# Kernel tuning notes

Hardware: AMD Instinct MI355X
Metric: run time of the kernel (lower is better)

## Reference

```python
import jax, jax.numpy as jnp
import numpy as np

# config constants (init_kwargs)
WC, WS = 0.5, 0.5            # boundary cosine / structural weights (hybrid mode)
TARGET_BPP = 6.0             # target_bytes_per_patch
GAIN = 1.0                   # target_patch_gain
THRESH = 0.5                 # boundary_threshold; mask = p >= THRESH
EPS = 1e-6

_POP6 = jnp.array([bin(i).count('1') for i in range(64)], dtype=jnp.int32)

def _pop6(x):
    return _POP6[jnp.clip(x, 0, 63)]

def _logit(p):
    p = jnp.clip(p, EPS, 1.0 - EPS)
    return jnp.log(p) - jnp.log1p(-p)

def _next(x):  # shift-left by one, zero-padded at end (matches torch q_next pattern)
    return jnp.concatenate([x[1:], jnp.zeros((1,), x.dtype)])

def _hist(vals, mask, bins):
    idx = jnp.where(mask, vals, bins)  # invalid -> out of range, dropped
    return jnp.zeros((bins,), jnp.int32).at[idx].add(1, mode='drop')


def setup_inputs() -> dict:
    key = jax.random.key(0)
    ks = jax.random.split(key, 6)
    B, S = 4, 1048576
    return {
        'boundary_logprobs': jax.random.normal(ks[0], (B, S), jnp.float32),
        'states': jax.random.randint(ks[1], (B, S), 0, 4096, jnp.int32),
        'q_class': jax.random.randint(ks[2], (B, S), 0, 64, jnp.int32),
        'family': jax.random.randint(ks[3], (B, S), 0, 4, jnp.int32),
        'micro_ref': jax.random.randint(ks[4], (B, S), 0, 64, jnp.int32),
        'valid_mask': jax.random.randint(ks[5], (B, S), 0, 2, jnp.int32).astype(bool),
    }


def reference(boundary_logprobs, states, q_class, family, micro_ref, valid_mask):
    B, S = valid_mask.shape
    v = valid_mask.reshape(-1)
    st = states.reshape(-1).astype(jnp.int32)
    q = q_class.reshape(-1).astype(jnp.int32)
    fam = family.reshape(-1).astype(jnp.int32)
    mic = micro_ref.reshape(-1).astype(jnp.int32)

    # --- structural boundary probs ---
    omega12 = st & 0xFFF
    c6 = ((omega12 >> 6) ^ omega12) & 63          # chirality6
    d_chi = jnp.clip(_pop6(c6 ^ _next(c6)).astype(jnp.float32) / 6.0, 0.0, 1.0)
    d_q = _pop6((q & 63) ^ (_next(q) & 63)).astype(jnp.float32) / 6.0
    fx = (fam & 3) ^ (_next(fam) & 3)
    d_fam = (((fx & 1) != 0).astype(jnp.float32) + ((fx & 2) != 0).astype(jnp.float32)) / 2.0
    score = jnp.clip(0.5 * d_chi + 0.35 * d_q + 0.15 * d_fam, EPS, 1.0)
    structural = jnp.where(v, score, 0.0)

    # --- combine with cosine probs (hybrid mode) ---
    cosine = jnp.exp(jnp.minimum(boundary_logprobs.reshape(-1), 0.0))
    combined = (WC * cosine + WS * structural) / max(WC + WS, 1e-6)

    # --- target bytes-per-patch rate adjustment ---
    vf = v.astype(jnp.float32)
    vc = jnp.maximum(jnp.sum(vf), 1.0)
    cur = jnp.clip(jnp.sum(combined * vf) / vc, 1e-4, 1.0 - 1e-4)
    tgt = max(1e-4, min(1.0 - 1e-4, 1.0 / TARGET_BPP))
    shift = _logit(jnp.asarray(tgt, jnp.float32)) - _logit(cur)
    combined = jax.nn.sigmoid(_logit(combined) + GAIN * shift)
    combined = jnp.clip(combined, EPS, 1.0 - EPS)
    combined_logprobs = jnp.log(combined)
    bmask = combined_logprobs >= jnp.log(jnp.asarray(THRESH, jnp.float32))

    # --- histograms over effective (valid) positions ---
    shell = _pop6(c6)
    q_hist64 = _hist(q, v, 64)
    family_hist4 = _hist(fam, v, 4)
    micro_hist64 = _hist(mic, v, 64)
    shell_hist7 = _hist(shell, v, 7)
    wt_q = _pop6(q & 63)
    q_weight_hist7 = _hist(wt_q, v, 7)
    bits = ((q & 63)[:, None] >> jnp.arange(6)) & 1            # [n, 6]
    bit_excitation6 = jnp.sum(bits * v[:, None].astype(jnp.int32), axis=0)

    # --- patch lengths (vectorized run-length over valid bytes) ---
    bv = bmask & v
    pos = jnp.cumsum(v.astype(jnp.int32))                      # 1-indexed valid position
    bpos = jnp.where(bv, pos, 0)
    prev = jax.lax.cummax(jnp.concatenate([jnp.zeros((1,), jnp.int32), bpos[:-1]]))
    lengths = jnp.where(bv, pos - prev, 0)                     # dense run lengths at boundaries
    total_valid = pos[-1]
    trailing = total_valid - jax.lax.cummax(bpos)[-1]          # open trailing run
    patch_count = jnp.sum(bv).astype(jnp.int32) + (trailing > 0).astype(jnp.int32)

    return (combined_logprobs.reshape(B, S), bmask.reshape(B, S), structural.reshape(B, S),
            q_hist64, family_hist4, micro_hist64, shell_hist7, q_weight_hist7,
            bit_excitation6, lengths, trailing, patch_count)
```

## Files before the change

kernel.cpp:

```cpp
#include <hip/hip_runtime.h>

#define TPB 256
#define EPT 8
#define CHUNK (TPB * EPT)
#define NSLICE 64

typedef unsigned long long ull;
typedef long long ll;

__device__ __forceinline__ ull shfl_down_u64(ull x, int off) {
    unsigned lo = (unsigned)x, hi = (unsigned)(x >> 32);
    lo = __shfl_down(lo, off, 64);
    hi = __shfl_down(hi, off, 64);
    return ((ull)hi << 32) | lo;
}

__global__ __launch_bounds__(TPB, 8) void k_passA(
    const float* __restrict__ blp, const int* __restrict__ st,
    const int* __restrict__ q, const int* __restrict__ fam,
    const int* __restrict__ mic, const int* __restrict__ vm,
    float* __restrict__ out_structural,
    int* __restrict__ ghist, ull* __restrict__ lookA,
    int* __restrict__ pos_offset, float* __restrict__ shiftp,
    int* __restrict__ totalv_p, int n)
{
    __shared__ int lh2[2048];
    __shared__ int slhs[11];
    __shared__ int swv[4];
    __shared__ float swc[4];

    const int tid = threadIdx.x, lane = tid & 63, wave = tid >> 6;
    const long i0 = (long)blockIdx.x * CHUNK + (long)tid * EPT;
    const bool fast = ((long)(blockIdx.x + 1) * CHUNK <= n);

    int stv[9], qv[9], fv[9], micv[8], vmv[8];
    float bpv[8];
    if (fast) {
        const int4 sa = *(const int4*)(st + i0),  sb = *(const int4*)(st + i0 + 4);
        const int4 qa = *(const int4*)(q + i0),   qb = *(const int4*)(q + i0 + 4);
        const int4 fa = *(const int4*)(fam + i0), fb = *(const int4*)(fam + i0 + 4);
        const int4 ma = *(const int4*)(mic + i0), mb = *(const int4*)(mic + i0 + 4);
        const int4 va = *(const int4*)(vm + i0),  vb = *(const int4*)(vm + i0 + 4);
        const float4 ba = *(const float4*)(blp + i0), bb = *(const float4*)(blp + i0 + 4);
        int nst = __shfl_down(sa.x, 1, 64);
        int nq  = __shfl_down(qa.x, 1, 64);
        int nf  = __shfl_down(fa.x, 1, 64);
        if (lane == 63) {
            const long j = i0 + 8;
            nst = (j < n) ? st[j]  : 0;
            nq  = (j < n) ? q[j]   : 0;
            nf  = (j < n) ? fam[j] : 0;
        }
        stv[0]=sa.x; stv[1]=sa.y; stv[2]=sa.z; stv[3]=sa.w; stv[4]=sb.x; stv[5]=sb.y; stv[6]=sb.z; stv[7]=sb.w; stv[8]=nst;
        qv[0]=qa.x;  qv[1]=qa.y;  qv[2]=qa.z;  qv[3]=qa.w;  qv[4]=qb.x;  qv[5]=qb.y;  qv[6]=qb.z;  qv[7]=qb.w;  qv[8]=nq;
        fv[0]=fa.x;  fv[1]=fa.y;  fv[2]=fa.z;  fv[3]=fa.w;  fv[4]=fb.x;  fv[5]=fb.y;  fv[6]=fb.z;  fv[7]=fb.w;  fv[8]=nf;
        micv[0]=ma.x; micv[1]=ma.y; micv[2]=ma.z; micv[3]=ma.w; micv[4]=mb.x; micv[5]=mb.y; micv[6]=mb.z; micv[7]=mb.w;
        vmv[0]=va.x; vmv[1]=va.y; vmv[2]=va.z; vmv[3]=va.w; vmv[4]=vb.x; vmv[5]=vb.y; vmv[6]=vb.z; vmv[7]=vb.w;
        bpv[0]=ba.x; bpv[1]=ba.y; bpv[2]=ba.z; bpv[3]=ba.w; bpv[4]=bb.x; bpv[5]=bb.y; bpv[6]=bb.z; bpv[7]=bb.w;
    } else {
        #pragma unroll
        for (int e = 0; e < 8; ++e) {
            long ii = i0 + e;
            bool r = ii < n;
            stv[e] = r ? st[ii] : 0;  qv[e] = r ? q[ii] : 0;  fv[e] = r ? fam[ii] : 0;
            micv[e] = r ? mic[ii] : 0; vmv[e] = r ? vm[ii] : 0; bpv[e] = r ? blp[ii] : 0.f;
        }
        stv[8] = (i0 + 8 < n) ? st[i0 + 8] : 0;
        qv[8]  = (i0 + 8 < n) ? q[i0 + 8] : 0;
        fv[8]  = (i0 + 8 < n) ? fam[i0 + 8] : 0;
    }

    {
        int4 z4; z4.x = 0; z4.y = 0; z4.z = 0; z4.w = 0;
        *(int4*)&lh2[tid * 8] = z4;
        *(int4*)&lh2[tid * 8 + 4] = z4;
    }
    if (tid < 11) slhs[tid] = 0;
    __syncthreads();

    const int qrow = ((wave << 2) | (lane & 3)) << 6;
    int sv = 0;
    float scf = 0.0f;
    ull accF = 0, accS0 = 0, accS1 = 0;
    float structural[8];
    #pragma unroll
    for (int e = 0; e < 8; ++e) {
        int sti = stv[e], qi = qv[e], fi = fv[e], mi = micv[e];
        int v = (vmv[e] != 0);
        int om  = sti & 0xFFF;      int c6  = ((om  >> 6) ^ om ) & 63;
        int omn = stv[e+1] & 0xFFF; int c6n = ((omn >> 6) ^ omn) & 63;
        float d_chi = (float)__popc(c6 ^ c6n) * (1.0f / 6.0f);
        float d_q   = (float)__popc((qi & 63) ^ (qv[e+1] & 63)) * (1.0f / 6.0f);
        int fx = (fi & 3) ^ (fv[e+1] & 3);
        float d_fam = (float)((fx & 1) + ((fx >> 1) & 1)) * 0.5f;
        float score = 0.5f * d_chi + 0.35f * d_q + 0.15f * d_fam;
        score = fminf(fmaxf(score, 1e-6f), 1.0f);
        structural[e] = v ? score : 0.0f;
        float cosine = expf(fminf(bpv[e], 0.0f));
        float combined = 0.5f * (cosine + structural[e]);
        if (v) {
            sv += 1;
            scf += combined;
            atomicAdd(&lh2[qrow + (qi & 63)], 1);
            atomicAdd(&lh2[1024 + qrow + (mi & 63)], 1);
            accF += 1ULL << ((fi & 3) * 16);
            int sh = __popc(c6);
            ull ts = 1ULL << ((sh & 3) * 16);
            if (sh < 4) accS0 += ts; else accS1 += ts;
        }
    }

    if (fast) {
        float4 o;
        o.x=structural[0]; o.y=structural[1]; o.z=structural[2]; o.w=structural[3];
        *(float4*)(out_structural + i0) = o;
        o.x=structural[4]; o.y=structural[5]; o.z=structural[6]; o.w=structural[7];
        *(float4*)(out_structural + i0 + 4) = o;
    } else {
        #pragma unroll
        for (int e = 0; e < 8; ++e)
            if (i0 + e < n) out_structural[i0 + e] = structural[e];
    }

    #pragma unroll
    for (int off = 32; off > 0; off >>= 1) {
        sv  += __shfl_down(sv, off, 64);
        scf += __shfl_down(scf, off, 64);
        accF  += shfl_down_u64(accF, off);
        accS0 += shfl_down_u64(accS0, off);
        accS1 += shfl_down_u64(accS1, off);
    }
    if (lane == 0) {
        swv[wave] = sv; swc[wave] = scf;
        #pragma unroll
        for (int b2 = 0; b2 < 4; ++b2) atomicAdd(&slhs[b2],     (int)((accF  >> (16*b2)) & 0xFFFF));
        #pragma unroll
        for (int b2 = 0; b2 < 4; ++b2) atomicAdd(&slhs[4 + b2], (int)((accS0 >> (16*b2)) & 0xFFFF));
        #pragma unroll
        for (int b2 = 0; b2 < 3; ++b2) atomicAdd(&slhs[8 + b2], (int)((accS1 >> (16*b2)) & 0xFFFF));
    }
    __syncthreads();

    if (wave != 0) {
        int t2 = tid - 64;
        if (t2 < 139) {
            int val;
            if (t2 < 64) {
                val = 0;
                #pragma unroll
                for (int r = 0; r < 16; ++r) val += lh2[(r << 6) + t2];
            } else if (t2 < 68) {
                val = slhs[t2 - 64];
            } else if (t2 < 132) {
                int b2 = t2 - 68;
                val = 0;
                #pragma unroll
                for (int r = 0; r < 16; ++r) val += lh2[1024 + (r << 6) + b2];
            } else {
                val = slhs[4 + (t2 - 132)];
            }
            if (val) atomicAdd(&ghist[(blockIdx.x & (NSLICE - 1)) * 152 + t2], val);
        }
    } else {
        const int b = blockIdx.x;
        const ll lv = (ll)(swv[0] + swv[1] + swv[2] + swv[3]);
        const double lcd = (double)swc[0] + (double)swc[1] + (double)swc[2] + (double)swc[3];
        const ll lcf = (ll)(lcd * 16384.0 + 0.5);
        if (lane == 0)
            atomicExch(&lookA[b], (1ULL << 62) | ((ull)lv << 39) | (ull)lcf);
        ll exV = 0, exC = 0;
        int base = b - 1;
        while (base >= 0) {
            int idx = base - lane;
            ull w; int stt;
            for (;;) {
                w = (idx >= 0) ? atomicAdd(&lookA[idx], 0ULL) : (2ULL << 62);
                stt = (int)(w >> 62);
                if (!__ballot(stt == 0)) break;
                __builtin_amdgcn_s_sleep(1);
            }
            ull incm = __ballot(stt == 2);
            int stop = incm ? (__ffsll((ll)incm) - 1) : 64;
            ll v = 0, c = 0;
            if (lane <= stop && idx >= 0) {
                v = (ll)((w >> 39) & 0x7FFFFFULL);
                c = (ll)(w & 0x7FFFFFFFFFULL);
            }
            #pragma unroll
            for (int off = 32; off > 0; off >>= 1) {
                v += (ll)shfl_down_u64((ull)v, off);
                c += (ll)shfl_down_u64((ull)c, off);
            }
            exV += v; exC += c;
            if (stop < 64) break;
            base -= 64;
        }
        if (lane == 0) {
            atomicExch(&lookA[b], (2ULL << 62) | ((ull)(exV + lv) << 39) | (ull)(exC + lcf));
            pos_offset[b] = (int)exV;
            if (b == (int)gridDim.x - 1) {
                int tv = (int)(exV + lv);
                *totalv_p = tv;
                double vc = (double)(tv > 1 ? tv : 1);
                float cur = (float)(((double)(exC + lcf) * (1.0 / 16384.0)) / vc);
                cur = fminf(fmaxf(cur, 1e-4f), 0.9999f);
                float p = fminf(fmaxf(cur, 1e-6f), 0.999999f);
                float lc = logf(p) - log1pf(-p);
                float tgt = (float)(1.0 / 6.0);
                float lt = logf(tgt) - log1pf(-tgt);
                *shiftp = lt - lc;
            }
        }
    }
}

__global__ __launch_bounds__(TPB, 8) void k_passB(
    const float* __restrict__ strc, const float* __restrict__ blp,
    const int* __restrict__ pos_offset, const float* __restrict__ shiftp,
    const int* __restrict__ totalv_p, const int* __restrict__ ghist,
    ull* __restrict__ lookB,
    float* __restrict__ out_logp, float* __restrict__ out_bmask,
    float* __restrict__ out_len, float* __restrict__ out_hist,
    float* __restrict__ out_trailing, float* __restrict__ out_patch, int n)
{
    __shared__ int swt[4], swm[4], scnt[4];
    __shared__ int sCarry;
    __shared__ int qh[64];
    const int tid = threadIdx.x, lane = tid & 63, wave = tid >> 6;
    const long i0 = (long)blockIdx.x * CHUNK + (long)tid * EPT;
    const bool fast = ((long)(blockIdx.x + 1) * CHUNK <= n);

    float sv8[8], bp8[8];
    if (fast) {
        const float4 s0 = *(const float4*)(strc + i0), s1 = *(const float4*)(strc + i0 + 4);
        const float4 p0 = *(const float4*)(blp + i0),  p1 = *(const float4*)(blp + i0 + 4);
        sv8[0]=s0.x; sv8[1]=s0.y; sv8[2]=s0.z; sv8[3]=s0.w; sv8[4]=s1.x; sv8[5]=s1.y; sv8[6]=s1.z; sv8[7]=s1.w;
        bp8[0]=p0.x; bp8[1]=p0.y; bp8[2]=p0.z; bp8[3]=p0.w; bp8[4]=p1.x; bp8[5]=p1.y; bp8[6]=p1.z; bp8[7]=p1.w;
    } else {
        #pragma unroll
        for (int e = 0; e < 8; ++e) {
            long ii = i0 + e;
            bool r = ii < n;
            sv8[e] = r ? strc[ii] : 0.0f;
            bp8[e] = r ? blp[ii] : 0.0f;
        }
    }

    const float shift = *shiftp;
    const int wb0 = pos_offset[blockIdx.x];
    const float K = expf(-shift);

    unsigned mv = 0, mb = 0;
    float lp[8], bmf[8], lenv[8];
    #pragma unroll
    for (int e = 0; e < 8; ++e) {
        float s = sv8[e];
        int v = (s > 0.0f);
        float cosine = expf(fminf(bp8[e], 0.0f));
        float comb = 0.5f * (cosine + s);
        float p = fminf(fmaxf(comb, 1e-6f), 0.999999f);
        float d = fmaf(K, 1.0f - p, p);
        float sgm = p / d;
        sgm = fminf(fmaxf(sgm, 1e-6f), 0.999999f);
        float clp = logf(sgm);
        lp[e] = clp;
        int bm = (clp >= -0.69314718f) ? 1 : 0;
        bmf[e] = (float)bm;
        mv |= (unsigned)v << e;
        if (bm & v) mb |= 1u << e;
        lenv[e] = 0.0f;
    }
    if (fast) {
        float4 o;
        o.x=lp[0]; o.y=lp[1]; o.z=lp[2]; o.w=lp[3];     *(float4*)(out_logp + i0) = o;
        o.x=lp[4]; o.y=lp[5]; o.z=lp[6]; o.w=lp[7];     *(float4*)(out_logp + i0 + 4) = o;
        o.x=bmf[0]; o.y=bmf[1]; o.z=bmf[2]; o.w=bmf[3]; *(float4*)(out_bmask + i0) = o;
        o.x=bmf[4]; o.y=bmf[5]; o.z=bmf[6]; o.w=bmf[7]; *(float4*)(out_bmask + i0 + 4) = o;
    } else {
        #pragma unroll
        for (int e = 0; e < 8; ++e)
            if (i0 + e < n) { out_logp[i0 + e] = lp[e]; out_bmask[i0 + e] = bmf[e]; }
    }

    int tvc = __popc(mv);
    int x = tvc;
    #pragma unroll
    for (int off = 1; off < 64; off <<= 1) {
        int y = __shfl_up(x, off, 64);
        if (lane >= off) x += y;
    }
    if (lane == 63) swt[wave] = x;
    __syncthreads();
    int wb = wb0;
    for (int w2 = 0; w2 < wave; ++w2) wb += swt[w2];
    const int vbase = wb + (x - tvc);

    int last = -1;
    if (mb) {
        int hb = 31 - __clz(mb);
        last = vbase + __popc(mv & ((2u << hb) - 1));
    }
    int m = last;
    #pragma unroll
    for (int off = 1; off < 64; off <<= 1) {
        int y = __shfl_up(m, off, 64);
        if (lane >= off && y > m) m = y;
    }
    int exm = __shfl_up(m, 1, 64);
    if (lane == 0) exm = -1;
    if (lane == 63) swm[wave] = m;
    int cnt = __popc(mb);
    #pragma unroll
    for (int off = 32; off > 0; off >>= 1)
        cnt += __shfl_down(cnt, off, 64);
    if (lane == 0) scnt[wave] = cnt;
    __syncthreads();

    if (wave == 0) {
        const int b = blockIdx.x;
        int Lown = swm[0];
        if (swm[1] > Lown) Lown = swm[1];
        if (swm[2] > Lown) Lown = swm[2];
        if (swm[3] > Lown) Lown = swm[3];
        if (Lown < 0) Lown = 0;
        const ll Cown = (ll)(scnt[0] + scnt[1] + scnt[2] + scnt[3]);
        if (lane == 0)
            atomicExch(&lookB[b], (1ULL << 62) | ((ull)Lown << 23) | (ull)Cown);
        ll exM = 0, exC = 0;
        int base = b - 1;
        while (base >= 0) {
            int idx = base - lane;
            ull w; int stt;
            for (;;) {
                w = (idx >= 0) ? atomicAdd(&lookB[idx], 0ULL) : (2ULL << 62);
                stt = (int)(w >> 62);
                if (!__ballot(stt == 0)) break;
                __builtin_amdgcn_s_sleep(1);
            }
            ull incm = __ballot(stt == 2);
            int stop = incm ? (__ffsll((ll)incm) - 1) : 64;
            ll mm = 0, c = 0;
            if (lane <= stop && idx >= 0) {
                mm = (ll)((w >> 23) & 0x7FFFFFULL);
                c  = (ll)(w & 0x7FFFFFULL);
            }
            #pragma unroll
            for (int off = 32; off > 0; off >>= 1) {
                ll mo = (ll)shfl_down_u64((ull)mm, off);
                if (mo > mm) mm = mo;
                c += (ll)shfl_down_u64((ull)c, off);
            }
            if (mm > exM) exM = mm;
            exC += c;
            if (stop < 64) break;
            base -= 64;
        }
        if (lane == 0) {
            ll incM = exM > (ll)Lown ? exM : (ll)Lown;
            atomicExch(&lookB[b], (2ULL << 62) | ((ull)incM << 23) | (ull)(exC + Cown));
            sCarry = (int)exM;
            if (b == (int)gridDim.x - 1) {
                int tv = *totalv_p;
                int trailing = tv - (int)incM;
                *out_trailing = (float)trailing;
                *out_patch = (float)((int)(exC + Cown) + (trailing > 0 ? 1 : 0));
            }
        }
    }
    __syncthreads();

    int prev = sCarry;
    if (exm > prev) prev = exm;
    for (int w2 = 0; w2 < wave; ++w2) if (swm[w2] > prev) prev = swm[w2];
    int runv = 0;
    #pragma unroll
    for (int e = 0; e < 8; ++e) {
        runv += (mv >> e) & 1;
        if ((mb >> e) & 1) {
            int pos = vbase + runv;
            lenv[e] = (float)(pos - prev);
            prev = pos;
        }
    }
    if (fast) {
        float4 o;
        o.x=lenv[0]; o.y=lenv[1]; o.z=lenv[2]; o.w=lenv[3]; *(float4*)(out_len + i0) = o;
        o.x=lenv[4]; o.y=lenv[5]; o.z=lenv[6]; o.w=lenv[7]; *(float4*)(out_len + i0 + 4) = o;
    } else {
        #pragma unroll
        for (int e = 0; e < 8; ++e)
            if (i0 + e < n) out_len[i0 + e] = lenv[e];
    }

    if (blockIdx.x == 0) {
        if (tid < 139) {
            int acc = 0;
            #pragma unroll 8
            for (int sl = 0; sl < NSLICE; ++sl) acc += ghist[sl * 152 + tid];
            out_hist[tid] = (float)acc;
            if (tid < 64) qh[tid] = acc;
        }
        __syncthreads();
        if (tid < 7) {
            int sacc = 0;
            for (int b = 0; b < 64; ++b) if (__popc(b) == tid) sacc += qh[b];
            out_hist[139 + tid] = (float)sacc;
        }
        if (tid < 6) {
            int sacc = 0;
            for (int b = 0; b < 64; ++b) sacc += qh[b] * ((b >> tid) & 1);
            out_hist[146 + tid] = (float)sacc;
        }
    }
}

extern "C" void kernel_launch(void* const* d_in, const int* in_sizes, int n_in,
                              void* d_out, int out_size, void* d_ws, size_t ws_size,
                              hipStream_t stream)
{
    const float* blp = (const float*)d_in[0];
    const int* st   = (const int*)d_in[1];
    const int* q    = (const int*)d_in[2];
    const int* fam  = (const int*)d_in[3];
    const int* mic  = (const int*)d_in[4];
    const int* vm   = (const int*)d_in[5];
    const int n = in_sizes[0];
    const int nb = (n + CHUNK - 1) / CHUNK;

    float* out = (float*)d_out;
    float* out_logp       = out;
    float* out_bmask      = out + (size_t)n;
    float* out_structural = out + 2 * (size_t)n;
    float* out_hist       = out + 3 * (size_t)n;
    float* out_len        = out + 3 * (size_t)n + 152;
    float* out_trailing   = out + 4 * (size_t)n + 152;
    float* out_patch      = out + 4 * (size_t)n + 153;

    char* w = (char*)d_ws;
    int*    ghist      = (int*)(w);
    ull*    lookA      = (ull*)(w + 40960);
    ull*    lookB      = (ull*)(w + 57344);
    int*    pos_offset = (int*)(w + 73728);
    float*  shiftp     = (float*)(w + 81920);
    int*    totalv_p   = (int*)(w + 81924);

    hipMemsetAsync(w, 0, 73728, stream);

    k_passA<<<dim3(nb), dim3(TPB), 0, stream>>>(
        blp, st, q, fam, mic, vm, out_structural,
        ghist, lookA, pos_offset, shiftp, totalv_p, n);

    k_passB<<<dim3(nb), dim3(TPB), 0, stream>>>(
        out_structural, blp, pos_offset, shiftp, totalv_p, ghist, lookB,
        out_logp, out_bmask, out_len, out_hist, out_trailing, out_patch, n);
}
```

Baseline: 192.9 us.

## Replace decoupled look-back scans with two-level group aggregates and resize blocks

Pass A's serial decoupled look-back is replaced. Each block now writes a packed per-block partial and atomically adds it into a per-group (32-block) sum. Pass B computes its valid-position offset and the global shift directly from those group sums and in-group partials, so the inter-block chain in pass A goes away. Pass B's max/count scan now uses per-group atomicMax/atomicAdd with a done counter plus in-group partials instead of walking back through lookB. Blocks change from 256 threads × 8 elements to 512 × 4. This cuts the serialized look-back latency, but pass B still spins on other blocks, and it relies on the grid having at most 64 groups.

```diff
diff --git a/kernel.cpp b/kernel.cpp
--- a/kernel.cpp
+++ b/kernel.cpp
@@ -1,9 +1,10 @@
 #include <hip/hip_runtime.h>
 
-#define TPB 256
-#define EPT 8
+#define TPB 512
+#define EPT 4
 #define CHUNK (TPB * EPT)
 #define NSLICE 64
+#define NW 8
 
 typedef unsigned long long ull;
 typedef long long ll;
@@ -20,71 +21,69 @@
     const int* __restrict__ q, const int* __restrict__ fam,
     const int* __restrict__ mic, const int* __restrict__ vm,
     float* __restrict__ out_structural,
-    int* __restrict__ ghist, ull* __restrict__ lookA,
-    int* __restrict__ pos_offset, float* __restrict__ shiftp,
-    int* __restrict__ totalv_p, int n)
+    int* __restrict__ ghist, ull* __restrict__ partialA,
+    ull* __restrict__ l1sumA, int n)
 {
     __shared__ int lh2[2048];
     __shared__ int slhs[11];
-    __shared__ int swv[4];
-    __shared__ float swc[4];
+    __shared__ int swv[NW];
+    __shared__ float swc[NW];
 
     const int tid = threadIdx.x, lane = tid & 63, wave = tid >> 6;
     const long i0 = (long)blockIdx.x * CHUNK + (long)tid * EPT;
     const bool fast = ((long)(blockIdx.x + 1) * CHUNK <= n);
 
-    int stv[9], qv[9], fv[9], micv[8], vmv[8];
-    float bpv[8];
+    int stv[5], qv[5], fv[5], micv[4], vmv[4];
+    float bpv[4];
     if (fast) {
-        const int4 sa = *(const int4*)(st + i0),  sb = *(const int4*)(st + i0 + 4);
-        const int4 qa = *(const int4*)(q + i0),   qb = *(const int4*)(q + i0 + 4);
-        const int4 fa = *(const int4*)(fam + i0), fb = *(const int4*)(fam + i0 + 4);
-        const int4 ma = *(const int4*)(mic + i0), mb = *(const int4*)(mic + i0 + 4);
-        const int4 va = *(const int4*)(vm + i0),  vb = *(const int4*)(vm + i0 + 4);
-        const float4 ba = *(const float4*)(blp + i0), bb = *(const float4*)(blp + i0 + 4);
+        const int4 sa = *(const int4*)(st + i0);
+        const int4 qa = *(const int4*)(q + i0);
+        const int4 fa = *(const int4*)(fam + i0);
+        const int4 ma = *(const int4*)(mic + i0);
+        const int4 va = *(const int4*)(vm + i0);
+        const float4 ba = *(const float4*)(blp + i0);
         int nst = __shfl_down(sa.x, 1, 64);
         int nq  = __shfl_down(qa.x, 1, 64);
         int nf  = __shfl_down(fa.x, 1, 64);
         if (lane == 63) {
-            const long j = i0 + 8;
+            const long j = i0 + 4;
             nst = (j < n) ? st[j]  : 0;
             nq  = (j < n) ? q[j]   : 0;
             nf  = (j < n) ? fam[j] : 0;
         }
-        stv[0]=sa.x; stv[1]=sa.y; stv[2]=sa.z; stv[3]=sa.w; stv[4]=sb.x; stv[5]=sb.y; stv[6]=sb.z; stv[7]=sb.w; stv[8]=nst;
-        qv[0]=qa.x;  qv[1]=qa.y;  qv[2]=qa.z;  qv[3]=qa.w;  qv[4]=qb.x;  qv[5]=qb.y;  qv[6]=qb.z;  qv[7]=qb.w;  qv[8]=nq;
-        fv[0]=fa.x;  fv[1]=fa.y;  fv[2]=fa.z;  fv[3]=fa.w;  fv[4]=fb.x;  fv[5]=fb.y;  fv[6]=fb.z;  fv[7]=fb.w;  fv[8]=nf;
-        micv[0]=ma.x; micv[1]=ma.y; micv[2]=ma.z; micv[3]=ma.w; micv[4]=mb.x; micv[5]=mb.y; micv[6]=mb.z; micv[7]=mb.w;
-        vmv[0]=va.x; vmv[1]=va.y; vmv[2]=va.z; vmv[3]=va.w; vmv[4]=vb.x; vmv[5]=vb.y; vmv[6]=vb.z; vmv[7]=vb.w;
-        bpv[0]=ba.x; bpv[1]=ba.y; bpv[2]=ba.z; bpv[3]=ba.w; bpv[4]=bb.x; bpv[5]=bb.y; bpv[6]=bb.z; bpv[7]=bb.w;
+        stv[0]=sa.x; stv[1]=sa.y; stv[2]=sa.z; stv[3]=sa.w; stv[4]=nst;
+        qv[0]=qa.x;  qv[1]=qa.y;  qv[2]=qa.z;  qv[3]=qa.w;  qv[4]=nq;
+        fv[0]=fa.x;  fv[1]=fa.y;  fv[2]=fa.z;  fv[3]=fa.w;  fv[4]=nf;
+        micv[0]=ma.x; micv[1]=ma.y; micv[2]=ma.z; micv[3]=ma.w;
+        vmv[0]=va.x; vmv[1]=va.y; vmv[2]=va.z; vmv[3]=va.w;
+        bpv[0]=ba.x; bpv[1]=ba.y; bpv[2]=ba.z; bpv[3]=ba.w;
     } else {
         #pragma unroll
-        for (int e = 0; e < 8; ++e) {
+        for (int e = 0; e < 4; ++e) {
             long ii = i0 + e;
             bool r = ii < n;
             stv[e] = r ? st[ii] : 0;  qv[e] = r ? q[ii] : 0;  fv[e] = r ? fam[ii] : 0;
             micv[e] = r ? mic[ii] : 0; vmv[e] = r ? vm[ii] : 0; bpv[e] = r ? blp[ii] : 0.f;
         }
-        stv[8] = (i0 + 8 < n) ? st[i0 + 8] : 0;
-        qv[8]  = (i0 + 8 < n) ? q[i0 + 8] : 0;
-        fv[8]  = (i0 + 8 < n) ? fam[i0 + 8] : 0;
+        stv[4] = (i0 + 4 < n) ? st[i0 + 4] : 0;
+        qv[4]  = (i0 + 4 < n) ? q[i0 + 4] : 0;
+        fv[4]  = (i0 + 4 < n) ? fam[i0 + 4] : 0;
     }
 
     {
         int4 z4; z4.x = 0; z4.y = 0; z4.z = 0; z4.w = 0;
-        *(int4*)&lh2[tid * 8] = z4;
-        *(int4*)&lh2[tid * 8 + 4] = z4;
+        *(int4*)&lh2[tid * 4] = z4;
     }
     if (tid < 11) slhs[tid] = 0;
     __syncthreads();
 
-    const int qrow = ((wave << 2) | (lane & 3)) << 6;
+    const int qrow = ((wave << 1) | (lane & 1)) << 6;
     int sv = 0;
     float scf = 0.0f;
     ull accF = 0, accS0 = 0, accS1 = 0;
-    float structural[8];
-    #pragma unroll
-    for (int e = 0; e < 8; ++e) {
+    float structural[4];
+    #pragma unroll
+    for (int e = 0; e < 4; ++e) {
         int sti = stv[e], qi = qv[e], fi = fv[e], mi = micv[e];
         int v = (vmv[e] != 0);
         int om  = sti & 0xFFF;      int c6  = ((om  >> 6) ^ om ) & 63;
@@ -114,11 +113,9 @@
         float4 o;
         o.x=structural[0]; o.y=structural[1]; o.z=structural[2]; o.w=structural[3];
         *(float4*)(out_structural + i0) = o;
-        o.x=structural[4]; o.y=structural[5]; o.z=structural[6]; o.w=structural[7];
-        *(float4*)(out_structural + i0 + 4) = o;
     } else {
         #pragma unroll
-        for (int e = 0; e < 8; ++e)
+        for (int e = 0; e < 4; ++e)
             if (i0 + e < n) out_structural[i0 + e] = structural[e];
     }
 
@@ -141,122 +138,109 @@
     }
     __syncthreads();
 
-    if (wave != 0) {
-        int t2 = tid - 64;
-        if (t2 < 139) {
-            int val;
-            if (t2 < 64) {
-                val = 0;
-                #pragma unroll
-                for (int r = 0; r < 16; ++r) val += lh2[(r << 6) + t2];
-            } else if (t2 < 68) {
-                val = slhs[t2 - 64];
-            } else if (t2 < 132) {
-                int b2 = t2 - 68;
-                val = 0;
-                #pragma unroll
-                for (int r = 0; r < 16; ++r) val += lh2[1024 + (r << 6) + b2];
-            } else {
-                val = slhs[4 + (t2 - 132)];
-            }
-            if (val) atomicAdd(&ghist[(blockIdx.x & (NSLICE - 1)) * 152 + t2], val);
-        }
-    } else {
-        const int b = blockIdx.x;
-        const ll lv = (ll)(swv[0] + swv[1] + swv[2] + swv[3]);
-        const double lcd = (double)swc[0] + (double)swc[1] + (double)swc[2] + (double)swc[3];
-        const ll lcf = (ll)(lcd * 16384.0 + 0.5);
-        if (lane == 0)
-            atomicExch(&lookA[b], (1ULL << 62) | ((ull)lv << 39) | (ull)lcf);
-        ll exV = 0, exC = 0;
-        int base = b - 1;
-        while (base >= 0) {
-            int idx = base - lane;
-            ull w; int stt;
-            for (;;) {
-                w = (idx >= 0) ? atomicAdd(&lookA[idx], 0ULL) : (2ULL << 62);
-                stt = (int)(w >> 62);
-                if (!__ballot(stt == 0)) break;
-                __builtin_amdgcn_s_sleep(1);
-            }
-            ull incm = __ballot(stt == 2);
-            int stop = incm ? (__ffsll((ll)incm) - 1) : 64;
-            ll v = 0, c = 0;
-            if (lane <= stop && idx >= 0) {
-                v = (ll)((w >> 39) & 0x7FFFFFULL);
-                c = (ll)(w & 0x7FFFFFFFFFULL);
-            }
+    if (tid == 0) {
+        int vsum = 0; double cs = 0.0;
+        #pragma unroll
+        for (int w2 = 0; w2 < NW; ++w2) { vsum += swv[w2]; cs += (double)swc[w2]; }
+        ll cf = (ll)(cs * 16384.0 + 0.5);
+        ull packed = ((ull)(unsigned)vsum << 39) | (ull)cf;
+        partialA[blockIdx.x] = packed;
+        atomicAdd(&l1sumA[blockIdx.x >> 5], packed);
+    }
+    if (tid < 139) {
+        int t2 = tid;
+        int val;
+        if (t2 < 64) {
+            val = 0;
             #pragma unroll
-            for (int off = 32; off > 0; off >>= 1) {
-                v += (ll)shfl_down_u64((ull)v, off);
-                c += (ll)shfl_down_u64((ull)c, off);
-            }
-            exV += v; exC += c;
-            if (stop < 64) break;
-            base -= 64;
-        }
-        if (lane == 0) {
-            atomicExch(&lookA[b], (2ULL << 62) | ((ull)(exV + lv) << 39) | (ull)(exC + lcf));
-            pos_offset[b] = (int)exV;
-            if (b == (int)gridDim.x - 1) {
-                int tv = (int)(exV + lv);
-                *totalv_p = tv;
-                double vc = (double)(tv > 1 ? tv : 1);
-                float cur = (float)(((double)(exC + lcf) * (1.0 / 16384.0)) / vc);
-                cur = fminf(fmaxf(cur, 1e-4f), 0.9999f);
-                float p = fminf(fmaxf(cur, 1e-6f), 0.999999f);
-                float lc = logf(p) - log1pf(-p);
-                float tgt = (float)(1.0 / 6.0);
-                float lt = logf(tgt) - log1pf(-tgt);
-                *shiftp = lt - lc;
-            }
-        }
+            for (int r = 0; r < 16; ++r) val += lh2[(r << 6) + t2];
+        } else if (t2 < 68) {
+            val = slhs[t2 - 64];
+        } else if (t2 < 132) {
+            int b2 = t2 - 68;
+            val = 0;
+            #pragma unroll
+            for (int r = 0; r < 16; ++r) val += lh2[1024 + (r << 6) + b2];
+        } else {
+            val = slhs[4 + (t2 - 132)];
+        }
+        if (val) atomicAdd(&ghist[(blockIdx.x & (NSLICE - 1)) * 152 + t2], val);
     }
 }
 
 __global__ __launch_bounds__(TPB, 8) void k_passB(
     const float* __restrict__ strc, const float* __restrict__ blp,
-    const int* __restrict__ pos_offset, const float* __restrict__ shiftp,
-    const int* __restrict__ totalv_p, const int* __restrict__ ghist,
-    ull* __restrict__ lookB,
+    const ull* __restrict__ partialA, const ull* __restrict__ l1sumA,
+    const int* __restrict__ ghist,
+    ull* __restrict__ partial2, unsigned* __restrict__ l1max2,
+    unsigned* __restrict__ l1cnt2, int* __restrict__ grpdone2,
     float* __restrict__ out_logp, float* __restrict__ out_bmask,
     float* __restrict__ out_len, float* __restrict__ out_hist,
     float* __restrict__ out_trailing, float* __restrict__ out_patch, int n)
 {
-    __shared__ int swt[4], swm[4], scnt[4];
-    __shared__ int sCarry;
+    __shared__ int swt[NW], swm[NW], scnt[NW];
+    __shared__ int sCarry, sTV, sPos0;
+    __shared__ float sShift;
     __shared__ int qh[64];
     const int tid = threadIdx.x, lane = tid & 63, wave = tid >> 6;
     const long i0 = (long)blockIdx.x * CHUNK + (long)tid * EPT;
     const bool fast = ((long)(blockIdx.x + 1) * CHUNK <= n);
-
-    float sv8[8], bp8[8];
+    const int nb = (int)gridDim.x;
+    const int b = (int)blockIdx.x;
+    const int g = b >> 5, r = b & 31;
+
+    float sv4[4], bp4[4];
     if (fast) {
-        const float4 s0 = *(const float4*)(strc + i0), s1 = *(const float4*)(strc + i0 + 4);
-        const float4 p0 = *(const float4*)(blp + i0),  p1 = *(const float4*)(blp + i0 + 4);
-        sv8[0]=s0.x; sv8[1]=s0.y; sv8[2]=s0.z; sv8[3]=s0.w; sv8[4]=s1.x; sv8[5]=s1.y; sv8[6]=s1.z; sv8[7]=s1.w;
-        bp8[0]=p0.x; bp8[1]=p0.y; bp8[2]=p0.z; bp8[3]=p0.w; bp8[4]=p1.x; bp8[5]=p1.y; bp8[6]=p1.z; bp8[7]=p1.w;
+        const float4 s0 = *(const float4*)(strc + i0);
+        const float4 p0 = *(const float4*)(blp + i0);
+        sv4[0]=s0.x; sv4[1]=s0.y; sv4[2]=s0.z; sv4[3]=s0.w;
+        bp4[0]=p0.x; bp4[1]=p0.y; bp4[2]=p0.z; bp4[3]=p0.w;
     } else {
         #pragma unroll
-        for (int e = 0; e < 8; ++e) {
+        for (int e = 0; e < 4; ++e) {
             long ii = i0 + e;
-            bool r = ii < n;
-            sv8[e] = r ? strc[ii] : 0.0f;
-            bp8[e] = r ? blp[ii] : 0.0f;
-        }
-    }
-
-    const float shift = *shiftp;
-    const int wb0 = pos_offset[blockIdx.x];
+            bool r2 = ii < n;
+            sv4[e] = r2 ? strc[ii] : 0.0f;
+            bp4[e] = r2 ? blp[ii] : 0.0f;
+        }
+    }
+
+    if (wave == 0) {
+        ull cell = l1sumA[lane];
+        int vc = (int)(cell >> 39);
+        ll cc = (ll)(cell & ((1ULL << 39) - 1));
+        int vex = (lane < g) ? vc : 0;
+        if (lane < r) vex += (int)(partialA[(g << 5) + lane] >> 39);
+        int vt = vc; ll ct = cc;
+        #pragma unroll
+        for (int off = 32; off > 0; off >>= 1) {
+            vt  += __shfl_down(vt, off, 64);
+            vex += __shfl_down(vex, off, 64);
+            ct  += (ll)shfl_down_u64((ull)ct, off);
+        }
+        if (lane == 0) {
+            sTV = vt; sPos0 = vex;
+            double vcd = (double)(vt > 1 ? vt : 1);
+            float cur = (float)(((double)ct * (1.0 / 16384.0)) / vcd);
+            cur = fminf(fmaxf(cur, 1e-4f), 0.9999f);
+            float p = fminf(fmaxf(cur, 1e-6f), 0.999999f);
+            float lc = logf(p) - log1pf(-p);
+            float tgt = (float)(1.0 / 6.0);
+            float lt = logf(tgt) - log1pf(-tgt);
+            sShift = lt - lc;
+        }
+    }
+    __syncthreads();
+    const float shift = sShift;
     const float K = expf(-shift);
 
     unsigned mv = 0, mb = 0;
-    float lp[8], bmf[8], lenv[8];
-    #pragma unroll
-    for (int e = 0; e < 8; ++e) {
-        float s = sv8[e];
+    float lp[4], bmf[4], lenv[4];
+    #pragma unroll
+    for (int e = 0; e < 4; ++e) {
+        float s = sv4[e];
         int v = (s > 0.0f);
-        float cosine = expf(fminf(bp8[e], 0.0f));
+        float cosine = expf(fminf(bp4[e], 0.0f));
         float comb = 0.5f * (cosine + s);
         float p = fminf(fmaxf(comb, 1e-6f), 0.999999f);
         float d = fmaf(K, 1.0f - p, p);
@@ -273,12 +257,10 @@
     if (fast) {
         float4 o;
         o.x=lp[0]; o.y=lp[1]; o.z=lp[2]; o.w=lp[3];     *(float4*)(out_logp + i0) = o;
-        o.x=lp[4]; o.y=lp[5]; o.z=lp[6]; o.w=lp[7];     *(float4*)(out_logp + i0 + 4) = o;
         o.x=bmf[0]; o.y=bmf[1]; o.z=bmf[2]; o.w=bmf[3]; *(float4*)(out_bmask + i0) = o;
-        o.x=bmf[4]; o.y=bmf[5]; o.z=bmf[6]; o.w=bmf[7]; *(float4*)(out_bmask + i0 + 4) = o;
     } else {
         #pragma unroll
-        for (int e = 0; e < 8; ++e)
+        for (int e = 0; e < 4; ++e)
             if (i0 + e < n) { out_logp[i0 + e] = lp[e]; out_bmask[i0 + e] = bmf[e]; }
     }
 
@@ -291,7 +273,7 @@
     }
     if (lane == 63) swt[wave] = x;
     __syncthreads();
-    int wb = wb0;
+    int wb = sPos0;
     for (int w2 = 0; w2 < wave; ++w2) wb += swt[w2];
     const int vbase = wb + (x - tvc);
 
@@ -317,53 +299,52 @@
     __syncthreads();
 
     if (wave == 0) {
-        const int b = blockIdx.x;
-        int Lown = swm[0];
-        if (swm[1] > Lown) Lown = swm[1];
-        if (swm[2] > Lown) Lown = swm[2];
-        if (swm[3] > Lown) Lown = swm[3];
+        int Lown = swm[0], Cown = scnt[0];
+        #pragma unroll
+        for (int w2 = 1; w2 < NW; ++w2) {
+            if (swm[w2] > Lown) Lown = swm[w2];
+            Cown += scnt[w2];
+        }
         if (Lown < 0) Lown = 0;
-        const ll Cown = (ll)(scnt[0] + scnt[1] + scnt[2] + scnt[3]);
-        if (lane == 0)
-            atomicExch(&lookB[b], (1ULL << 62) | ((ull)Lown << 23) | (ull)Cown);
-        ll exM = 0, exC = 0;
-        int base = b - 1;
-        while (base >= 0) {
-            int idx = base - lane;
-            ull w; int stt;
-            for (;;) {
-                w = (idx >= 0) ? atomicAdd(&lookB[idx], 0ULL) : (2ULL << 62);
-                stt = (int)(w >> 62);
-                if (!__ballot(stt == 0)) break;
-                __builtin_amdgcn_s_sleep(1);
-            }
-            ull incm = __ballot(stt == 2);
-            int stop = incm ? (__ffsll((ll)incm) - 1) : 64;
-            ll mm = 0, c = 0;
-            if (lane <= stop && idx >= 0) {
-                mm = (ll)((w >> 23) & 0x7FFFFFULL);
-                c  = (ll)(w & 0x7FFFFFULL);
-            }
-            #pragma unroll
-            for (int off = 32; off > 0; off >>= 1) {
-                ll mo = (ll)shfl_down_u64((ull)mm, off);
-                if (mo > mm) mm = mo;
-                c += (ll)shfl_down_u64((ull)c, off);
-            }
-            if (mm > exM) exM = mm;
-            exC += c;
-            if (stop < 64) break;
-            base -= 64;
-        }
         if (lane == 0) {
-            ll incM = exM > (ll)Lown ? exM : (ll)Lown;
-            atomicExch(&lookB[b], (2ULL << 62) | ((ull)incM << 23) | (ull)(exC + Cown));
-            sCarry = (int)exM;
-            if (b == (int)gridDim.x - 1) {
-                int tv = *totalv_p;
-                int trailing = tv - (int)incM;
+            atomicExch(&partial2[b],
+                       (1ULL << 63) | ((ull)(unsigned)Lown << 23) | (ull)(unsigned)Cown);
+            atomicMax(&l1max2[g], (unsigned)Lown);
+            atomicAdd(&l1cnt2[g], (unsigned)Cown);
+            asm volatile("s_waitcnt vmcnt(0)" ::: "memory");
+            atomicAdd(&grpdone2[g], 1);
+        }
+        const bool needG = (lane < g);
+        const bool needP = (lane < r);
+        int tgtc = 32;
+        if (needG) { int t2 = nb - (lane << 5); tgtc = t2 < 32 ? t2 : 32; }
+        ull pw = 0;
+        for (;;) {
+            bool okG = true, okP = true;
+            if (needG) okG = (atomicAdd(&grpdone2[lane], 0) >= tgtc);
+            if (needP) { pw = atomicAdd(&partial2[(g << 5) + lane], 0ULL); okP = (pw >> 63) != 0; }
+            if (__all(okG && okP)) break;
+            __builtin_amdgcn_s_sleep(4);
+        }
+        unsigned gm = needG ? atomicAdd(&l1max2[lane], 0u) : 0u;
+        unsigned gc = needG ? atomicAdd(&l1cnt2[lane], 0u) : 0u;
+        unsigned pm = needP ? (unsigned)((pw >> 23) & 0x7FFFFFu) : 0u;
+        unsigned pc = needP ? (unsigned)(pw & 0x7FFFFFu) : 0u;
+        unsigned em = gm > pm ? gm : pm;
+        unsigned ec = gc + pc;
+        #pragma unroll
+        for (int off = 32; off > 0; off >>= 1) {
+            unsigned y = __shfl_down(em, off, 64);
+            if (y > em) em = y;
+            ec += __shfl_down(ec, off, 64);
+        }
+        if (lane == 0) {
+            sCarry = (int)em;
+            if (b == nb - 1) {
+                int inclM = (int)em > Lown ? (int)em : Lown;
+                int trailing = sTV - inclM;
                 *out_trailing = (float)trailing;
-                *out_patch = (float)((int)(exC + Cown) + (trailing > 0 ? 1 : 0));
+                *out_patch = (float)((int)ec + Cown + (trailing > 0 ? 1 : 0));
             }
         }
     }
@@ -374,7 +355,7 @@
     for (int w2 = 0; w2 < wave; ++w2) if (swm[w2] > prev) prev = swm[w2];
     int runv = 0;
     #pragma unroll
-    for (int e = 0; e < 8; ++e) {
+    for (int e = 0; e < 4; ++e) {
         runv += (mv >> e) & 1;
         if ((mb >> e) & 1) {
             int pos = vbase + runv;
@@ -385,14 +366,13 @@
     if (fast) {
         float4 o;
         o.x=lenv[0]; o.y=lenv[1]; o.z=lenv[2]; o.w=lenv[3]; *(float4*)(out_len + i0) = o;
-        o.x=lenv[4]; o.y=lenv[5]; o.z=lenv[6]; o.w=lenv[7]; *(float4*)(out_len + i0 + 4) = o;
     } else {
         #pragma unroll
-        for (int e = 0; e < 8; ++e)
+        for (int e = 0; e < 4; ++e)
             if (i0 + e < n) out_len[i0 + e] = lenv[e];
     }
 
-    if (blockIdx.x == 0) {
+    if (b == 0) {
         if (tid < 139) {
             int acc = 0;
             #pragma unroll 8
@@ -403,12 +383,12 @@
         __syncthreads();
         if (tid < 7) {
             int sacc = 0;
-            for (int b = 0; b < 64; ++b) if (__popc(b) == tid) sacc += qh[b];
+            for (int bb = 0; bb < 64; ++bb) if (__popc(bb) == tid) sacc += qh[bb];
             out_hist[139 + tid] = (float)sacc;
         }
         if (tid < 6) {
             int sacc = 0;
-            for (int b = 0; b < 64; ++b) sacc += qh[b] * ((b >> tid) & 1);
+            for (int bb = 0; bb < 64; ++bb) sacc += qh[bb] * ((bb >> tid) & 1);
             out_hist[146 + tid] = (float)sacc;
         }
     }
@@ -437,20 +417,22 @@
     float* out_patch      = out + 4 * (size_t)n + 153;
 
     char* w = (char*)d_ws;
-    int*    ghist      = (int*)(w);
-    ull*    lookA      = (ull*)(w + 40960);
-    ull*    lookB      = (ull*)(w + 57344);
-    int*    pos_offset = (int*)(w + 73728);
-    float*  shiftp     = (float*)(w + 81920);
-    int*    totalv_p   = (int*)(w + 81924);
-
-    hipMemsetAsync(w, 0, 73728, stream);
+    int*      ghist    = (int*)(w);
+    ull*      l1sumA   = (ull*)(w + 38912);
+    unsigned* l1max2   = (unsigned*)(w + 39424);
+    unsigned* l1cnt2   = (unsigned*)(w + 39680);
+    int*      grpdone2 = (int*)(w + 39936);
+    ull*      partial2 = (ull*)(w + 40960);
+    ull*      partialA = (ull*)(w + 57344);
+
+    hipMemsetAsync(w, 0, 57344, stream);
 
     k_passA<<<dim3(nb), dim3(TPB), 0, stream>>>(
         blp, st, q, fam, mic, vm, out_structural,
-        ghist, lookA, pos_offset, shiftp, totalv_p, n);
+        ghist, partialA, l1sumA, n);
 
     k_passB<<<dim3(nb), dim3(TPB), 0, stream>>>(
-        out_structural, blp, pos_offset, shiftp, totalv_p, ghist, lookB,
+        out_structural, blp, partialA, l1sumA, ghist,
+        partial2, l1max2, l1cnt2, grpdone2,
         out_logp, out_bmask, out_len, out_hist, out_trailing, out_patch, n);
 }
```

After: 267.9 us. 1.39x slower.
